# Kernel optimization log

Measured on AMD Instinct MI355X. Metric: run time of the kernel, lower is better.

Reference implementation:

```python
import jax, jax.numpy as jnp
import numpy as np

H = 128
W = 128
FX = 128.0
FY = 128.0
CX = 64.0
CY = 64.0
EPS = 1e-8  # added to den once per gaussian chunk, as in the original


def quat2mat(q):
    q = q / jnp.linalg.norm(q)
    w, x, y, z = q[0], q[1], q[2], q[3]
    return jnp.stack([
        jnp.stack([1 - 2 * (y * y + z * z), 2 * (x * y - z * w), 2 * (x * z + y * w)]),
        jnp.stack([2 * (x * y + z * w), 1 - 2 * (x * x + z * z), 2 * (y * z - x * w)]),
        jnp.stack([2 * (x * z - y * w), 2 * (y * z + x * w), 1 - 2 * (x * x + y * y)]),
    ])


def setup_inputs() -> dict:
    key = jax.random.key(0)
    ks = jax.random.split(key, 7)
    N = 16384
    # camera-space-ish positions: z in [2,6], x/y scaled so projections land on-screen
    z = jax.random.uniform(ks[0], (N, 1), minval=2.0, maxval=6.0)
    xy = jax.random.uniform(ks[1], (N, 2), minval=-0.45, maxval=0.45) * z
    positions = jnp.concatenate([xy, z], axis=1)          # [N,3]
    colors = jax.random.uniform(ks[2], (N, 3))             # [N,3]
    opacities = jax.random.uniform(ks[3], (N, 1), minval=0.3, maxval=1.0)  # [N,1]
    scales = jax.random.uniform(ks[4], (N, 1), minval=3.0, maxval=15.0)    # [N,1], pixel units
    qvec = jnp.array([1.0, 0.0, 0.0, 0.0]) + 0.01 * jax.random.normal(ks[5], (4,))
    tvec = 0.01 * jax.random.normal(ks[6], (3,))
    return {"positions": positions, "colors": colors, "opacities": opacities,
            "scales": scales, "qvec": qvec, "tvec": tvec,
            "tile_hw": 64, "chunk_gauss": 8192}


def _render(positions, colors, opacities, scales, qvec, tvec, tile_hw, chunk_gauss):
    N = positions.shape[0]
    HWp = H * W
    R = quat2mat(qvec)
    cam = positions @ R.T + tvec[None, :]                    # [N,3] camera coords
    proj = jnp.stack([cam[:, 0] / cam[:, 2] * FX + CX,
                      cam[:, 1] / cam[:, 2] * FY + CY], axis=1)  # [N,2] screen (x,y)

    xs = jnp.arange(W, dtype=positions.dtype)
    ys = jnp.arange(H, dtype=positions.dtype)
    yy, xx = jnp.meshgrid(ys, xs, indexing='ij')
    pix = jnp.stack([xx.reshape(-1), yy.reshape(-1)], axis=1)  # [HW,2] (x,y), row-major

    var = scales[:, 0] ** 2                                   # [N] isotropic variance (px^2)

    n_chunks = N // chunk_gauss
    pj_c = proj.reshape(n_chunks, chunk_gauss, 2)
    cl_c = colors.reshape(n_chunks, chunk_gauss, 3)
    op_c = opacities.reshape(n_chunks, chunk_gauss, 1)
    var_c = var.reshape(n_chunks, chunk_gauss)

    def body(carry, chunk):
        num, den = carry
        pj, cl, op, v = chunk
        diff = pix[None, :, :] - pj[:, None, :]               # [G,HW,2]
        dist2 = jnp.sum(diff * diff, axis=-1)                 # [G,HW]
        w = op * jnp.exp(-0.5 * dist2 / v[:, None])           # [G,HW] RBF weight * opacity
        num = num + jnp.einsum('gp,gc->pc', w, cl)            # [HW,3]
        den = den + jnp.sum(w, axis=0)[:, None] + EPS         # [HW,1]
        return (num, den), None

    init = (jnp.zeros((HWp, 3), positions.dtype), jnp.zeros((HWp, 1), positions.dtype))
    (num, den), _ = jax.lax.scan(body, init, (pj_c, cl_c, op_c, var_c))

    img = num / den                                           # [HW,3]
    step = tile_hw * tile_hw
    T = HWp // step
    # per tile: (acc_num/acc_den).t().reshape(3, tile_hw, tile_hw), stacked over tiles
    return img.reshape(T, step, 3).transpose(0, 2, 1).reshape(T, 3, tile_hw, tile_hw)


def reference(positions, colors, opacities, scales, qvec, tvec, tile_hw, chunk_gauss):
    return _render(positions, colors, opacities, scales, qvec, tvec, tile_hw, chunk_gauss)
```

## Files before the change

### kernel.cpp

```cpp
#include <hip/hip_runtime.h>

typedef _Float16 f16x8 __attribute__((ext_vector_type(8)));
typedef float    f32x4 __attribute__((ext_vector_type(4)));

#define W_IMG   128
#define H_IMG   128
#define HW_IMG  16384
#define FX_C    128.0f
#define FY_C    128.0f
#define CX_C    64.0f
#define CY_C    64.0f
#define LOG2E_F 1.4426950408889634f
#define SUPER   128
#define KCH     32

__device__ __forceinline__ float4 proj_of(
    const float* __restrict__ pos, const float* __restrict__ opac,
    const float* __restrict__ scl, const float* __restrict__ qv,
    const float* __restrict__ tv, int i)
{
    float qw = qv[0], qx = qv[1], qy = qv[2], qz = qv[3];
    float qn = sqrtf(qw*qw + qx*qx + qy*qy + qz*qz);
    qw /= qn; qx /= qn; qy /= qn; qz /= qn;

    float R00 = 1.f - 2.f*(qy*qy + qz*qz), R01 = 2.f*(qx*qy - qz*qw), R02 = 2.f*(qx*qz + qy*qw);
    float R10 = 2.f*(qx*qy + qz*qw), R11 = 1.f - 2.f*(qx*qx + qz*qz), R12 = 2.f*(qy*qz - qx*qw);
    float R20 = 2.f*(qx*qz - qy*qw), R21 = 2.f*(qy*qz + qx*qw), R22 = 1.f - 2.f*(qx*qx + qy*qy);

    float x = pos[3*i + 0];
    float y = pos[3*i + 1];
    float z = pos[3*i + 2];

    float cx = R00*x + R01*y + R02*z + tv[0];
    float cy = R10*x + R11*y + R12*z + tv[1];
    float cz = R20*x + R21*y + R22*z + tv[2];

    float px = cx / cz * FX_C + CX_C;
    float py = cy / cz * FY_C + CY_C;

    float s   = scl[i];
    float a2  = (-0.5f / (s * s)) * LOG2E_F;

    float4 r; r.x = px; r.y = py; r.z = a2; r.w = opac[i];
    return r;
}

__global__ __launch_bounds__(256, 2) void gemm_mfma(
    const float* __restrict__ pos, const float* __restrict__ col,
    const float* __restrict__ opac, const float* __restrict__ scl,
    const float* __restrict__ qv, const float* __restrict__ tv,
    float4* __restrict__ part, int segLen)
{
    __shared__ __align__(16) float4 Pa[SUPER];
    __shared__ __align__(16) float4 Pb[SUPER];

    int tid  = threadIdx.x;
    int lane = tid & 63;
    int wid  = tid >> 6;
    int li   = lane & 15;
    int kb   = lane >> 4;

    int xb = (blockIdx.x & 1) * 64 + (wid & 1) * 32;
    int yb = (blockIdx.x >> 1) * 64 + (wid >> 1) * 32;
    int g0 = blockIdx.y * segLen;

    f32x4 aR[2][2], aG[2][2], aB[2][2], aD[2][2];
    #pragma unroll
    for (int yt = 0; yt < 2; ++yt)
        #pragma unroll
        for (int xt = 0; xt < 2; ++xt) {
            aR[yt][xt] = (f32x4)0.f; aG[yt][xt] = (f32x4)0.f;
            aB[yt][xt] = (f32x4)0.f; aD[yt][xt] = (f32x4)0.f;
        }

    for (int s0 = 0; s0 < segLen; s0 += SUPER) {
        int sc = (segLen - s0 < SUPER) ? (segLen - s0) : SUPER;

        __syncthreads();
        if (tid < sc) {
            Pa[tid] = proj_of(pos, opac, scl, qv, tv, g0 + s0 + tid);
        } else if (tid >= 128) {
            for (int k = tid - 128; k < 3 * sc; k += 128) {
                int g  = k / 3;
                int ch = k - 3 * g;
                reinterpret_cast<float*>(Pb)[g * 4 + ch] =
                    col[3 * (g0 + s0 + g) + ch];
            }
        }
        __syncthreads();

        for (int c0 = 0; c0 < sc; c0 += KCH) {
            float px_[8], py_[8], a2_[8], op_[8], cr_[8], cg_[8], cb_[8];
            #pragma unroll
            for (int i = 0; i < 8; ++i) {
                int gg = c0 + kb * 8 + i;
                float4 a = Pa[gg];
                float4 b = Pb[gg];
                px_[i] = a.x; py_[i] = a.y; a2_[i] = a.z; op_[i] = a.w;
                cr_[i] = b.x; cg_[i] = b.y; cb_[i] = b.z;
            }

            f16x8 Bu[2];
            #pragma unroll
            for (int xt = 0; xt < 2; ++xt) {
                float X = (float)(xb + xt * 16 + li);
                #pragma unroll
                for (int i = 0; i < 8; ++i) {
                    float dx = X - px_[i];
                    float u  = op_[i] * __builtin_amdgcn_exp2f(a2_[i] * dx * dx);
                    Bu[xt][i] = (_Float16)u;
                }
            }

            #pragma unroll
            for (int yt = 0; yt < 2; ++yt) {
                float Y = (float)(yb + yt * 16 + li);
                f16x8 Ar, Ag, Ab2, Ad;
                #pragma unroll
                for (int i = 0; i < 8; ++i) {
                    float dy = Y - py_[i];
                    float v  = __builtin_amdgcn_exp2f(a2_[i] * dy * dy);
                    Ad[i]  = (_Float16)v;
                    Ar[i]  = (_Float16)(v * cr_[i]);
                    Ag[i]  = (_Float16)(v * cg_[i]);
                    Ab2[i] = (_Float16)(v * cb_[i]);
                }
                #pragma unroll
                for (int xt = 0; xt < 2; ++xt) {
                    aR[yt][xt] = __builtin_amdgcn_mfma_f32_16x16x32_f16(
                        Ar,  Bu[xt], aR[yt][xt], 0, 0, 0);
                    aG[yt][xt] = __builtin_amdgcn_mfma_f32_16x16x32_f16(
                        Ag,  Bu[xt], aG[yt][xt], 0, 0, 0);
                    aB[yt][xt] = __builtin_amdgcn_mfma_f32_16x16x32_f16(
                        Ab2, Bu[xt], aB[yt][xt], 0, 0, 0);
                    aD[yt][xt] = __builtin_amdgcn_mfma_f32_16x16x32_f16(
                        Ad,  Bu[xt], aD[yt][xt], 0, 0, 0);
                }
            }
        }
    }

    size_t segBase = (size_t)blockIdx.y * HW_IMG;
    #pragma unroll
    for (int yt = 0; yt < 2; ++yt)
        #pragma unroll
        for (int xt = 0; xt < 2; ++xt)
            #pragma unroll
            for (int i = 0; i < 4; ++i) {
                int y = yb + yt * 16 + kb * 4 + i;
                int x = xb + xt * 16 + li;
                float4 o;
                o.x = aR[yt][xt][i]; o.y = aG[yt][xt][i];
                o.z = aB[yt][xt][i]; o.w = aD[yt][xt][i];
                part[segBase + (size_t)y * 128 + x] = o;
            }
}

__global__ __launch_bounds__(256) void render_fb(
    const float* __restrict__ pos, const float* __restrict__ col,
    const float* __restrict__ opac, const float* __restrict__ scl,
    const float* __restrict__ qv, const float* __restrict__ tv,
    float4* __restrict__ part, int segLen)
{
    int p = blockIdx.x * 256 + threadIdx.x;
    float X = (float)(p & (W_IMG - 1));
    float Y = (float)(p >> 7);

    int g0 = blockIdx.y * segLen;
    float nr = 0.f, ng = 0.f, nb = 0.f, den = 0.f;
    for (int j = 0; j < segLen; ++j) {
        int g = g0 + j;
        float4 pg = proj_of(pos, opac, scl, qv, tv, g);
        float dx = X - pg.x;
        float dy = Y - pg.y;
        float d2 = fmaf(dx, dx, dy * dy);
        float e  = pg.w * __builtin_amdgcn_exp2f(pg.z * d2);
        nr  = fmaf(e, col[3*g+0], nr);
        ng  = fmaf(e, col[3*g+1], ng);
        nb  = fmaf(e, col[3*g+2], nb);
        den += e;
    }
    float4 o; o.x = nr; o.y = ng; o.z = nb; o.w = den;
    part[(size_t)blockIdx.y * HW_IMG + p] = o;
}

__global__ __launch_bounds__(256) void finalize_kernel(
    const float4* __restrict__ part, float* __restrict__ out,
    const int* __restrict__ chunk_gauss_p, const int* __restrict__ tile_hw_p,
    int N, int nseg)
{
    int p = blockIdx.x * 256 + threadIdx.x;

    float nr = 0.f, ng = 0.f, nb = 0.f, den = 0.f;
    #pragma unroll 8
    for (int s = 0; s < nseg; ++s) {
        float4 v = part[(size_t)s * HW_IMG + p];
        nr += v.x; ng += v.y; nb += v.z; den += v.w;
    }

    int cg = chunk_gauss_p[0];
    int n_chunks = (cg > 0) ? (N / cg) : 0;
    den += (float)n_chunks * 1e-8f;

    int th   = tile_hw_p[0];
    int step = th * th;
    if (step <= 0 || step > HW_IMG) { th = 64; step = th * th; }
    int t  = p / step;
    int s2 = p - t * step;
    size_t base = (size_t)t * 3 * step + s2;

    out[base]            = nr / den;
    out[base + step]     = ng / den;
    out[base + 2 * step] = nb / den;
}

extern "C" void kernel_launch(void* const* d_in, const int* in_sizes, int n_in,
                              void* d_out, int out_size, void* d_ws, size_t ws_size,
                              hipStream_t stream)
{
    const float* pos  = (const float*)d_in[0];
    const float* col  = (const float*)d_in[1];
    const float* opac = (const float*)d_in[2];
    const float* scl  = (const float*)d_in[3];
    const float* qv   = (const float*)d_in[4];
    const float* tv   = (const float*)d_in[5];
    const int* tile_hw_p     = (const int*)d_in[6];
    const int* chunk_gauss_p = (const int*)d_in[7];

    int N = in_sizes[2];

    int S = 0;
    for (int cand = 128; cand >= 8; cand >>= 1) {
        if (N % cand == 0 && ((N / cand) % KCH) == 0 &&
            (size_t)cand * HW_IMG * 16 <= ws_size) { S = cand; break; }
    }

    float4* part = (float4*)d_ws;

    if (S > 0) {
        dim3 grid(4, S);
        gemm_mfma<<<grid, 256, 0, stream>>>(
            pos, col, opac, scl, qv, tv, part, N / S);

        finalize_kernel<<<HW_IMG / 256, 256, 0, stream>>>(
            part, (float*)d_out, chunk_gauss_p, tile_hw_p, N, S);
    } else {
        int nseg = 16;
        while (nseg > 1 &&
               ((size_t)nseg * HW_IMG * 16 > ws_size || (N % nseg) != 0))
            nseg >>= 1;

        dim3 grid(HW_IMG / 256, nseg);
        render_fb<<<grid, 256, 0, stream>>>(pos, col, opac, scl, qv, tv, part, N / nseg);

        finalize_kernel<<<HW_IMG / 256, 256, 0, stream>>>(
            part, (float*)d_out, chunk_gauss_p, tile_hw_p, N, nseg);
    }
}
```

Measured before the change: 94.79 us.

## Halve segment count, shrink warp tiles, and parallelize finalize segment reduction

Each warp in the MFMA kernel now covers a 32x16 pixel tile instead of 32x32, the grid doubles in x, and the number of gaussian segments is capped at 64 instead of 128. This halves the size of the partial-sum buffer written and read through global memory. The finalize kernel splits each pixel's segment sum across four threads and combines them in shared memory, launching four times more blocks. In exchange, the X-side exponentials are recomputed more often per gaussian, and each block does a longer serial loop.

```diff
diff --git a/kernel.cpp b/kernel.cpp
--- a/kernel.cpp
+++ b/kernel.cpp
@@ -61,17 +61,15 @@
     int kb   = lane >> 4;
 
     int xb = (blockIdx.x & 1) * 64 + (wid & 1) * 32;
-    int yb = (blockIdx.x >> 1) * 64 + (wid >> 1) * 32;
+    int yb = (blockIdx.x >> 1) * 32 + (wid >> 1) * 16;
     int g0 = blockIdx.y * segLen;
 
-    f32x4 aR[2][2], aG[2][2], aB[2][2], aD[2][2];
+    f32x4 aR[2], aG[2], aB[2], aD[2];
     #pragma unroll
-    for (int yt = 0; yt < 2; ++yt)
-        #pragma unroll
-        for (int xt = 0; xt < 2; ++xt) {
-            aR[yt][xt] = (f32x4)0.f; aG[yt][xt] = (f32x4)0.f;
-            aB[yt][xt] = (f32x4)0.f; aD[yt][xt] = (f32x4)0.f;
-        }
+    for (int xt = 0; xt < 2; ++xt) {
+        aR[xt] = (f32x4)0.f; aG[xt] = (f32x4)0.f;
+        aB[xt] = (f32x4)0.f; aD[xt] = (f32x4)0.f;
+    }
 
     for (int s0 = 0; s0 < segLen; s0 += SUPER) {
         int sc = (segLen - s0 < SUPER) ? (segLen - s0) : SUPER;
@@ -112,9 +110,8 @@
                 }
             }
 
-            #pragma unroll
-            for (int yt = 0; yt < 2; ++yt) {
-                float Y = (float)(yb + yt * 16 + li);
+            {
+                float Y = (float)(yb + li);
                 f16x8 Ar, Ag, Ab2, Ad;
                 #pragma unroll
                 for (int i = 0; i < 8; ++i) {
@@ -127,14 +124,14 @@
                 }
                 #pragma unroll
                 for (int xt = 0; xt < 2; ++xt) {
-                    aR[yt][xt] = __builtin_amdgcn_mfma_f32_16x16x32_f16(
-                        Ar,  Bu[xt], aR[yt][xt], 0, 0, 0);
-                    aG[yt][xt] = __builtin_amdgcn_mfma_f32_16x16x32_f16(
-                        Ag,  Bu[xt], aG[yt][xt], 0, 0, 0);
-                    aB[yt][xt] = __builtin_amdgcn_mfma_f32_16x16x32_f16(
-                        Ab2, Bu[xt], aB[yt][xt], 0, 0, 0);
-                    aD[yt][xt] = __builtin_amdgcn_mfma_f32_16x16x32_f16(
-                        Ad,  Bu[xt], aD[yt][xt], 0, 0, 0);
+                    aR[xt] = __builtin_amdgcn_mfma_f32_16x16x32_f16(
+                        Ar,  Bu[xt], aR[xt], 0, 0, 0);
+                    aG[xt] = __builtin_amdgcn_mfma_f32_16x16x32_f16(
+                        Ag,  Bu[xt], aG[xt], 0, 0, 0);
+                    aB[xt] = __builtin_amdgcn_mfma_f32_16x16x32_f16(
+                        Ab2, Bu[xt], aB[xt], 0, 0, 0);
+                    aD[xt] = __builtin_amdgcn_mfma_f32_16x16x32_f16(
+                        Ad,  Bu[xt], aD[xt], 0, 0, 0);
                 }
             }
         }
@@ -142,18 +139,16 @@
 
     size_t segBase = (size_t)blockIdx.y * HW_IMG;
     #pragma unroll
-    for (int yt = 0; yt < 2; ++yt)
+    for (int xt = 0; xt < 2; ++xt)
         #pragma unroll
-        for (int xt = 0; xt < 2; ++xt)
-            #pragma unroll
-            for (int i = 0; i < 4; ++i) {
-                int y = yb + yt * 16 + kb * 4 + i;
-                int x = xb + xt * 16 + li;
-                float4 o;
-                o.x = aR[yt][xt][i]; o.y = aG[yt][xt][i];
-                o.z = aB[yt][xt][i]; o.w = aD[yt][xt][i];
-                part[segBase + (size_t)y * 128 + x] = o;
-            }
+        for (int i = 0; i < 4; ++i) {
+            int y = yb + kb * 4 + i;
+            int x = xb + xt * 16 + li;
+            float4 o;
+            o.x = aR[xt][i]; o.y = aG[xt][i];
+            o.z = aB[xt][i]; o.w = aD[xt][i];
+            part[segBase + (size_t)y * 128 + x] = o;
+        }
 }
 
 __global__ __launch_bounds__(256) void render_fb(
@@ -189,29 +184,45 @@
     const int* __restrict__ chunk_gauss_p, const int* __restrict__ tile_hw_p,
     int N, int nseg)
 {
-    int p = blockIdx.x * 256 + threadIdx.x;
+    __shared__ float4 red[4][64];
+
+    int tid   = threadIdx.x;
+    int pxl   = tid & 63;
+    int lane4 = tid >> 6;
+    int p     = blockIdx.x * 64 + pxl;
 
     float nr = 0.f, ng = 0.f, nb = 0.f, den = 0.f;
-    #pragma unroll 8
-    for (int s = 0; s < nseg; ++s) {
+    for (int s = lane4; s < nseg; s += 4) {
         float4 v = part[(size_t)s * HW_IMG + p];
         nr += v.x; ng += v.y; nb += v.z; den += v.w;
     }
-
-    int cg = chunk_gauss_p[0];
-    int n_chunks = (cg > 0) ? (N / cg) : 0;
-    den += (float)n_chunks * 1e-8f;
-
-    int th   = tile_hw_p[0];
-    int step = th * th;
-    if (step <= 0 || step > HW_IMG) { th = 64; step = th * th; }
-    int t  = p / step;
-    int s2 = p - t * step;
-    size_t base = (size_t)t * 3 * step + s2;
-
-    out[base]            = nr / den;
-    out[base + step]     = ng / den;
-    out[base + 2 * step] = nb / den;
+    float4 a; a.x = nr; a.y = ng; a.z = nb; a.w = den;
+    red[lane4][pxl] = a;
+    __syncthreads();
+
+    if (tid < 64) {
+        float4 a0 = red[0][tid], a1 = red[1][tid], a2 = red[2][tid], a3 = red[3][tid];
+        float snr = (a0.x + a1.x) + (a2.x + a3.x);
+        float sng = (a0.y + a1.y) + (a2.y + a3.y);
+        float snb = (a0.z + a1.z) + (a2.z + a3.z);
+        float sd  = (a0.w + a1.w) + (a2.w + a3.w);
+
+        int cg = chunk_gauss_p[0];
+        int n_chunks = (cg > 0) ? (N / cg) : 0;
+        sd += (float)n_chunks * 1e-8f;
+
+        int th   = tile_hw_p[0];
+        int step = th * th;
+        if (step <= 0 || step > HW_IMG) { th = 64; step = th * th; }
+        int pp = blockIdx.x * 64 + tid;
+        int t  = pp / step;
+        int s2 = pp - t * step;
+        size_t base = (size_t)t * 3 * step + s2;
+
+        out[base]            = snr / sd;
+        out[base + step]     = sng / sd;
+        out[base + 2 * step] = snb / sd;
+    }
 }
 
 extern "C" void kernel_launch(void* const* d_in, const int* in_sizes, int n_in,
@@ -230,7 +241,7 @@
     int N = in_sizes[2];
 
     int S = 0;
-    for (int cand = 128; cand >= 8; cand >>= 1) {
+    for (int cand = 64; cand >= 8; cand >>= 1) {
         if (N % cand == 0 && ((N / cand) % KCH) == 0 &&
             (size_t)cand * HW_IMG * 16 <= ws_size) { S = cand; break; }
     }
@@ -238,11 +249,11 @@
     float4* part = (float4*)d_ws;
 
     if (S > 0) {
-        dim3 grid(4, S);
+        dim3 grid(8, S);
         gemm_mfma<<<grid, 256, 0, stream>>>(
             pos, col, opac, scl, qv, tv, part, N / S);
 
-        finalize_kernel<<<HW_IMG / 256, 256, 0, stream>>>(
+        finalize_kernel<<<HW_IMG / 64, 256, 0, stream>>>(
             part, (float*)d_out, chunk_gauss_p, tile_hw_p, N, S);
     } else {
         int nseg = 16;
@@ -253,7 +264,7 @@
         dim3 grid(HW_IMG / 256, nseg);
         render_fb<<<grid, 256, 0, stream>>>(pos, col, opac, scl, qv, tv, part, N / nseg);
 
-        finalize_kernel<<<HW_IMG / 256, 256, 0, stream>>>(
+        finalize_kernel<<<HW_IMG / 64, 256, 0, stream>>>(
             part, (float*)d_out, chunk_gauss_p, tile_hw_p, N, nseg);
     }
 }
```

New measurement: 89.69 us. 5.4% less time.
